# Kernel tuning notes

Hardware: AMD Instinct MI355X
Metric: run time of the kernel (lower is better)

## Reference

```python
import jax, jax.numpy as jnp
import numpy as np

# B complexes of L residues; C atom channels; K nearest neighbors
B, L, C, K = 8, 2500, 14, 9
N = B * L
E = N * K
NUM_CLASSES, EMB, HID, NL = 20, 128, 128, 3


def silu(x):
    return x * jax.nn.sigmoid(x)


def setup_inputs() -> dict:
    key = jax.random.key(0)
    ks = jax.random.split(key, 16)
    p = lambda k, shp, s=0.05: jax.random.normal(k, shp, dtype=jnp.float32) * s
    return {
        "X": jax.random.normal(ks[0], (N, C, 3), dtype=jnp.float32),
        "S": jax.random.randint(ks[1], (N,), 0, NUM_CLASSES),
        "E_tab": p(ks[2], (NUM_CLASSES, EMB)),       # residue embedding table
        "Wchan": p(ks[3], (NUM_CLASSES, C)),         # per-residue channel (atom) weights
        "Win": p(ks[4], (EMB, HID)),                 # input projection
        "Wr": p(ks[5], (NL, C * C, HID)),            # radial (channel-outer-product) projection
        "We1": p(ks[6], (NL, 3 * HID, HID)),         # edge MLP
        "be1": jnp.zeros((NL, HID), dtype=jnp.float32),
        "We2": p(ks[7], (NL, HID, HID)),
        "Wx1": p(ks[8], (NL, HID, HID)),             # coordinate-update MLP
        "Wx2": p(ks[9], (NL, HID, C), 0.01),
        "Wh1": p(ks[10], (NL, 2 * HID, HID)),        # node-update MLP
        "Wh2": p(ks[11], (NL, HID, HID)),
        "Wf1": p(ks[12], (HID, HID)),                # ffn_residue: SiLU,Linear,SiLU,Linear
        "Wf2": p(ks[13], (HID, NUM_CLASSES)),
    }


def knn_edges(X):
    # kNN graph per complex on CA (channel 1) coordinates, like _knn_edges
    pos = X[:, 1].reshape(B, L, 3)
    d2 = jnp.sum((pos[:, :, None, :] - pos[:, None, :, :]) ** 2, axis=-1)  # [B,L,L]
    d2 = d2 + jnp.eye(L, dtype=d2.dtype) * 1e9  # exclude self-edges
    _, idx = jax.lax.top_k(-d2, K)              # [B,L,K] nearest neighbors
    offs = (jnp.arange(B) * L)[:, None, None]
    dst = (idx + offs).reshape(-1)              # [E]
    src = jnp.repeat(jnp.arange(N), K)          # [E], sorted -> fast segment_sum
    return src, dst


def reference(X, S, E_tab, Wchan, Win, Wr, We1, be1, We2, Wx1, Wx2, Wh1, Wh2, Wf1, Wf2):
    src, dst = knn_edges(X)
    h = E_tab[S] @ Win                              # [N,HID]
    cw = jax.nn.softmax(Wchan[S], axis=-1)          # [N,C] channel weights
    cw_src = cw[src]                                # [E,C]
    for l in range(NL):
        xd = X[src] - X[dst]                        # [E,C,3]
        # MEAN-style channel-pair radial features
        rad = jnp.einsum("eci,edi->ecd", xd, xd).reshape(E, C * C) / C
        m = jnp.concatenate([h[src], h[dst], rad @ Wr[l]], axis=-1)
        m = silu(silu(m @ We1[l] + be1[l]) @ We2[l])           # [E,HID]
        coef = silu(m @ Wx1[l]) @ Wx2[l]                        # [E,C]
        xupd = xd * (coef * cw_src)[..., None]                  # [E,C,3]
        X = X + jax.ops.segment_sum(xupd, src, num_segments=N) / K
        aggm = jax.ops.segment_sum(m, src, num_segments=N)      # [N,HID]
        h = h + silu(jnp.concatenate([h, aggm], axis=-1) @ Wh1[l]) @ Wh2[l]
    # ffn_residue: Sequential(SiLU, Linear, SiLU, Linear)
    logits = silu(silu(h) @ Wf1) @ Wf2
    return logits, X
```

## Files before the change

### kernel.cpp

```cpp
#include <hip/hip_runtime.h>
#include <hip/hip_bf16.h>

typedef __hip_bfloat16 bf16;

constexpr int Bc  = 8;
constexpr int Lc  = 2500;
constexpr int Cc  = 14;
constexpr int Kc  = 9;
constexpr int Nn  = Bc * Lc;
constexpr int NCLS = 20;
constexpr int HID = 128;
constexpr int NL  = 3;
constexpr int CC  = Cc * Cc;
constexpr int X3  = Cc * 3;

typedef __bf16 bf16x8 __attribute__((ext_vector_type(8)));
typedef short  sh8    __attribute__((ext_vector_type(8)));
typedef float  f32x4  __attribute__((ext_vector_type(4)));

__device__ __forceinline__ float b2f(bf16 x) { return __bfloat162float(x); }
__device__ __forceinline__ float b2fu(unsigned short u) {
  return __uint_as_float(((unsigned int)u) << 16);
}
__device__ __forceinline__ unsigned short f2bu(float x) {
  bf16 h = __float2bfloat16(x);
  return *reinterpret_cast<unsigned short*>(&h);
}
__device__ __forceinline__ float siluf(float x) {
  return x * __builtin_amdgcn_rcpf(1.0f + __expf(-x));
}
__device__ __forceinline__ int clampi(int v, int n) {
  return ((unsigned)v < (unsigned)n) ? v : 0;
}
__device__ __forceinline__ void unpk2(unsigned int u, float& a, float& b) {
  a = __uint_as_float(u << 16);
  b = __uint_as_float(u & 0xffff0000u);
}

__device__ __forceinline__ f32x4 mfma16(sh8 a, sh8 b, f32x4 c) {
  return __builtin_amdgcn_mfma_f32_16x16x32_bf16(
      __builtin_bit_cast(bf16x8, a), __builtin_bit_cast(bf16x8, b), c, 0, 0, 0);
}

__device__ __forceinline__ int fragoff(int e, int k, int MT) {
  return (((k >> 5) * MT + (e >> 4)) << 9) +
         (((e & 15) + (((k >> 3) & 3) << 4)) << 3) + (k & 7);
}

__global__ __launch_bounds__(128) void wrp_kernel(const float* __restrict__ Wr,
                                                  const float* __restrict__ We1,
                                                  float* __restrict__ Wrp) {
  int l = blockIdx.x / CC, j = blockIdx.x % CC;
  int t = threadIdx.x;
  __shared__ float row[HID];
  row[t] = Wr[(size_t)(l * CC + j) * HID + t];
  __syncthreads();
  float acc = 0.f;
  #pragma unroll 4
  for (int k = 0; k < HID; ++k)
    acc += row[k] * We1[(size_t)(l * 384 + 256 + k) * HID + t];
  Wrp[(size_t)(l * CC + j) * HID + t] = acc;
}

constexpr int NSH = 26;
struct ShufArgs {
  const float* src[NSH];
  unsigned short* dst[NSH];
  int K[NSH], N[NSH], KT[NSH], NT[NSH];
};

__global__ void shufb_kernel(ShufArgs a) {
  int e = blockIdx.y;
  int K = a.K[e], N = a.N[e], NT = a.NT[e];
  int total = a.KT[e] * NT * 512;
  const float* W = a.src[e];
  unsigned short* out = a.dst[e];
  for (int idx = blockIdx.x * blockDim.x + threadIdx.x; idx < total;
       idx += gridDim.x * blockDim.x) {
    int j = idx & 7;
    int lane = (idx >> 3) & 63;
    int nt = (idx >> 9) % NT;
    int kt = idx / (512 * NT);
    int k = kt * 32 + ((lane >> 4) << 3) + j;
    int n = nt * 16 + (lane & 15);
    float v = (k < K && n < N) ? W[(size_t)k * N + n] : 0.f;
    out[idx] = f2bu(v);
  }
}

__global__ __launch_bounds__(128) void htab_kernel(const float* __restrict__ Et,
                                                   const float* __restrict__ Win,
                                                   const float* __restrict__ Wch,
                                                   float* __restrict__ Htab,
                                                   float* __restrict__ cwtab) {
  int r = blockIdx.x, t = threadIdx.x;
  __shared__ float e[HID];
  e[t] = Et[r * HID + t];
  __syncthreads();
  float acc = 0.f;
  #pragma unroll 4
  for (int k = 0; k < HID; ++k) acc += e[k] * Win[k * HID + t];
  Htab[r * HID + t] = acc;
  if (t == 0) {
    float v[Cc];
    float mx = -1e30f;
    for (int c = 0; c < Cc; ++c) { v[c] = Wch[r * Cc + c]; mx = fmaxf(mx, v[c]); }
    float s = 0.f;
    for (int c = 0; c < Cc; ++c) { v[c] = __expf(v[c] - mx); s += v[c]; }
    float inv = 1.0f / s;
    for (int c = 0; c < Cc; ++c) cwtab[r * Cc + c] = v[c] * inv;
  }
}

constexpr int PSTR = 2512;

__global__ void posx_kernel(const float* __restrict__ X, float* __restrict__ posG) {
  int total = Bc * PSTR;
  for (int i = blockIdx.x * blockDim.x + threadIdx.x; i < total;
       i += gridDim.x * blockDim.x) {
    int comp = i / PSTR, j = i - comp * PSTR;
    float x = 1e30f, y = 1e30f, z = 1e30f;
    if (j < Lc) {
      size_t g = (size_t)(comp * Lc + j) * X3;
      x = X[g + 3]; y = X[g + 4]; z = X[g + 5];
    }
    float* b = posG + (size_t)comp * 3 * PSTR;
    b[j] = x; b[PSTR + j] = y; b[2 * PSTR + j] = z;
  }
}

constexpr int KR2 = 8;
constexpr int KC2 = 80;

__global__ __launch_bounds__(256) void knn_kernel(const float* __restrict__ posG,
                                                  int* __restrict__ nbr) {
  constexpr int bpc = (Lc + KR2 - 1) / KR2;
  int comp = blockIdx.x / bpc, rb = blockIdx.x % bpc;
  int t = threadIdx.x;
  int rl = t >> 5, q = t & 31;
  int r = rb * KR2 + rl;
  const float* px = posG + (size_t)comp * 3 * PSTR;
  const float* py = px + PSTR;
  const float* pz = py + PSTR;

  float bd[Kc];
  int   bi[Kc];
  #pragma unroll
  for (int k = 0; k < Kc; ++k) { bd[k] = __int_as_float(0x7f800000); bi[k] = 0x7fffffff; }

  if (r < Lc) {
    float rx = px[r], ry = py[r], rz = pz[r];
    int c0 = q * KC2;
    int c1 = c0 + KC2; if (c1 > Lc) c1 = Lc;
    for (int i = c0; i < c1; i += 4) {
      float4 xs = *(const float4*)(px + i);
      float4 ys = *(const float4*)(py + i);
      float4 zs = *(const float4*)(pz + i);
      float d2v[4];
      {
        float dx, dy, dz;
        dx = rx - xs.x; dy = ry - ys.x; dz = rz - zs.x; d2v[0] = dx*dx + dy*dy + dz*dz;
        dx = rx - xs.y; dy = ry - ys.y; dz = rz - zs.y; d2v[1] = dx*dx + dy*dy + dz*dz;
        dx = rx - xs.z; dy = ry - ys.z; dz = rz - zs.z; d2v[2] = dx*dx + dy*dy + dz*dz;
        dx = rx - xs.w; dy = ry - ys.w; dz = rz - zs.w; d2v[3] = dx*dx + dy*dy + dz*dz;
      }
      #pragma unroll
      for (int u = 0; u < 4; ++u) {
        int ii = i + u;
        float d2 = d2v[u];
        if (ii != r && d2 < bd[Kc - 1]) {
          bd[Kc - 1] = d2; bi[Kc - 1] = ii;
          #pragma unroll
          for (int p = Kc - 1; p > 0; --p) {
            if (bd[p] < bd[p - 1]) {
              float td = bd[p]; bd[p] = bd[p - 1]; bd[p - 1] = td;
              int   ti = bi[p]; bi[p] = bi[p - 1]; bi[p - 1] = ti;
            }
          }
        }
      }
    }
  }

  int gbase = (comp * Lc + r) * Kc;
  #pragma unroll
  for (int k = 0; k < Kc; ++k) {
    unsigned long long mykey =
        ((unsigned long long)__float_as_uint(bd[0]) << 32) | (unsigned int)bi[0];
    unsigned long long w = mykey;
    #pragma unroll
    for (int m = 1; m <= 16; m <<= 1) {
      unsigned long long o = __shfl_xor(w, m);
      if (o < w) w = o;
    }
    if (r < Lc && q == k)
      nbr[gbase + k] = comp * Lc + (int)(unsigned int)(w & 0xffffffffULL);
    if (mykey == w) {
      #pragma unroll
      for (int s = 0; s < Kc - 1; ++s) { bd[s] = bd[s + 1]; bi[s] = bi[s + 1]; }
      bd[Kc - 1] = __int_as_float(0x7f800000); bi[Kc - 1] = 0x7fffffff;
    }
  }
}

__global__ __launch_bounds__(256) void nodeABm_kernel(
    const int* __restrict__ S, const float* __restrict__ Htab,
    float* __restrict__ hv,
    const unsigned short* __restrict__ We1a_s, const unsigned short* __restrict__ We1b_s,
    const float* __restrict__ be1n, bf16* __restrict__ hA, bf16* __restrict__ hB) {
  __shared__ __align__(16) unsigned short sB[4 * 512];
  int t = threadIdx.x, n0 = blockIdx.x * 16;
  int lane = t & 63, wv = t >> 6, quad = lane >> 4, l15 = lane & 15, wnb = wv << 5;

  for (int o = t; o < 16 * HID; o += 256) {
    int row = o >> 7, k = o & 127;
    float v = Htab[clampi(S[n0 + row], NCLS) * HID + k];
    hv[(size_t)(n0 + row) * HID + k] = v;
    sB[fragoff(row, k, 1)] = f2bu(v);
  }
  __syncthreads();

  f32x4 a3[2] = {{0,0,0,0},{0,0,0,0}}, a4[2] = {{0,0,0,0},{0,0,0,0}};
  const sh8* sBv = (const sh8*)sB;
  for (int kt = 0; kt < 4; ++kt) {
    sh8 a = sBv[kt * 64 + lane];
    sh8 b0 = ((const sh8*)We1a_s)[((kt << 3) + (wv << 1) + 0) * 64 + lane];
    sh8 b1 = ((const sh8*)We1a_s)[((kt << 3) + (wv << 1) + 1) * 64 + lane];
    sh8 c0 = ((const sh8*)We1b_s)[((kt << 3) + (wv << 1) + 0) * 64 + lane];
    sh8 c1 = ((const sh8*)We1b_s)[((kt << 3) + (wv << 1) + 1) * 64 + lane];
    a3[0] = mfma16(a, b0, a3[0]); a3[1] = mfma16(a, b1, a3[1]);
    a4[0] = mfma16(a, c0, a4[0]); a4[1] = mfma16(a, c1, a4[1]);
  }
  #pragma unroll
  for (int nl = 0; nl < 2; ++nl) {
    int col = wnb + (nl << 4) + l15;
    float be = be1n[col];
    #pragma unroll
    for (int r = 0; r < 4; ++r) {
      int row = (quad << 2) + r;
      hA[(size_t)(n0 + row) * HID + col] = __float2bfloat16(a3[nl][r] + be);
      hB[(size_t)(n0 + row) * HID + col] = __float2bfloat16(a4[nl][r]);
    }
  }
}

__global__ __launch_bounds__(256) void fupdAB_kernel(
    float* __restrict__ h, const bf16* __restrict__ aggm,
    const unsigned short* __restrict__ Wh1_s, const unsigned short* __restrict__ Wh2_s,
    const unsigned short* __restrict__ We1a_s, const unsigned short* __restrict__ We1b_s,
    const float* __restrict__ be1n, bf16* __restrict__ hA, bf16* __restrict__ hB) {
  __shared__ __align__(16) unsigned short sA[8 * 512];
  __shared__ __align__(16) unsigned short sB[4 * 512];
  int t = threadIdx.x, n0 = blockIdx.x * 16;
  int lane = t & 63, wv = t >> 6, quad = lane >> 4, l15 = lane & 15, wnb = wv << 5;

  for (int o = t; o < 16 * 256; o += 256) {
    int row = o >> 8, k = o & 255;
    float v = (k < HID) ? h[(size_t)(n0 + row) * HID + k]
                        : b2f(aggm[(size_t)(n0 + row) * HID + (k - HID)]);
    sA[fragoff(row, k, 1)] = f2bu(v);
  }
  __syncthreads();

  f32x4 a1[2] = {{0,0,0,0},{0,0,0,0}};
  const sh8* sAv = (const sh8*)sA;
  for (int kt = 0; kt < 8; ++kt) {
    sh8 a = sAv[kt * 64 + lane];
    sh8 b0 = ((const sh8*)Wh1_s)[((kt << 3) + (wv << 1) + 0) * 64 + lane];
    sh8 b1 = ((const sh8*)Wh1_s)[((kt << 3) + (wv << 1) + 1) * 64 + lane];
    a1[0] = mfma16(a, b0, a1[0]);
    a1[1] = mfma16(a, b1, a1[1]);
  }
  #pragma unroll
  for (int nl = 0; nl < 2; ++nl) {
    int col = wnb + (nl << 4) + l15;
    #pragma unroll
    for (int r = 0; r < 4; ++r)
      sB[fragoff((quad << 2) + r, col, 1)] = f2bu(siluf(a1[nl][r]));
  }
  __syncthreads();

  f32x4 a2[2] = {{0,0,0,0},{0,0,0,0}};
  const sh8* sBv = (const sh8*)sB;
  for (int kt = 0; kt < 4; ++kt) {
    sh8 a = sBv[kt * 64 + lane];
    sh8 b0 = ((const sh8*)Wh2_s)[((kt << 3) + (wv << 1) + 0) * 64 + lane];
    sh8 b1 = ((const sh8*)Wh2_s)[((kt << 3) + (wv << 1) + 1) * 64 + lane];
    a2[0] = mfma16(a, b0, a2[0]);
    a2[1] = mfma16(a, b1, a2[1]);
  }
  float hn[2][4];
  #pragma unroll
  for (int nl = 0; nl < 2; ++nl) {
    int col = wnb + (nl << 4) + l15;
    #pragma unroll
    for (int r = 0; r < 4; ++r) {
      int row = (quad << 2) + r;
      float v = h[(size_t)(n0 + row) * HID + col] + a2[nl][r];
      h[(size_t)(n0 + row) * HID + col] = v;
      hn[nl][r] = v;
    }
  }
  __syncthreads();
  #pragma unroll
  for (int nl = 0; nl < 2; ++nl) {
    int col = wnb + (nl << 4) + l15;
    #pragma unroll
    for (int r = 0; r < 4; ++r)
      sB[fragoff((quad << 2) + r, col, 1)] = f2bu(hn[nl][r]);
  }
  __syncthreads();

  f32x4 a3[2] = {{0,0,0,0},{0,0,0,0}}, a4[2] = {{0,0,0,0},{0,0,0,0}};
  for (int kt = 0; kt < 4; ++kt) {
    sh8 a = sBv[kt * 64 + lane];
    sh8 b0 = ((const sh8*)We1a_s)[((kt << 3) + (wv << 1) + 0) * 64 + lane];
    sh8 b1 = ((const sh8*)We1a_s)[((kt << 3) + (wv << 1) + 1) * 64 + lane];
    sh8 c0 = ((const sh8*)We1b_s)[((kt << 3) + (wv << 1) + 0) * 64 + lane];
    sh8 c1 = ((const sh8*)We1b_s)[((kt << 3) + (wv << 1) + 1) * 64 + lane];
    a3[0] = mfma16(a, b0, a3[0]); a3[1] = mfma16(a, b1, a3[1]);
    a4[0] = mfma16(a, c0, a4[0]); a4[1] = mfma16(a, c1, a4[1]);
  }
  #pragma unroll
  for (int nl = 0; nl < 2; ++nl) {
    int col = wnb + (nl << 4) + l15;
    float be = be1n[col];
    #pragma unroll
    for (int r = 0; r < 4; ++r) {
      int row = (quad << 2) + r;
      hA[(size_t)(n0 + row) * HID + col] = __float2bfloat16(a3[nl][r] + be);
      hB[(size_t)(n0 + row) * HID + col] = __float2bfloat16(a4[nl][r]);
    }
  }
}

__global__ __launch_bounds__(256) void fupdF_kernel(
    const float* __restrict__ h, const bf16* __restrict__ aggm,
    const unsigned short* __restrict__ Wh1_s, const unsigned short* __restrict__ Wh2_s,
    const unsigned short* __restrict__ Wf1_s, const unsigned short* __restrict__ Wf2_s,
    float* __restrict__ out) {
  __shared__ __align__(16) unsigned short sA[8 * 512];
  __shared__ __align__(16) unsigned short sB[4 * 512];
  int t = threadIdx.x, n0 = blockIdx.x * 16;
  int lane = t & 63, wv = t >> 6, quad = lane >> 4, l15 = lane & 15, wnb = wv << 5;

  for (int o = t; o < 16 * 256; o += 256) {
    int row = o >> 8, k = o & 255;
    float v = (k < HID) ? h[(size_t)(n0 + row) * HID + k]
                        : b2f(aggm[(size_t)(n0 + row) * HID + (k - HID)]);
    sA[fragoff(row, k, 1)] = f2bu(v);
  }
  __syncthreads();

  f32x4 a1[2] = {{0,0,0,0},{0,0,0,0}};
  const sh8* sAv = (const sh8*)sA;
  for (int kt = 0; kt < 8; ++kt) {
    sh8 a = sAv[kt * 64 + lane];
    sh8 b0 = ((const sh8*)Wh1_s)[((kt << 3) + (wv << 1) + 0) * 64 + lane];
    sh8 b1 = ((const sh8*)Wh1_s)[((kt << 3) + (wv << 1) + 1) * 64 + lane];
    a1[0] = mfma16(a, b0, a1[0]);
    a1[1] = mfma16(a, b1, a1[1]);
  }
  #pragma unroll
  for (int nl = 0; nl < 2; ++nl) {
    int col = wnb + (nl << 4) + l15;
    #pragma unroll
    for (int r = 0; r < 4; ++r)
      sB[fragoff((quad << 2) + r, col, 1)] = f2bu(siluf(a1[nl][r]));
  }
  __syncthreads();

  f32x4 a2[2] = {{0,0,0,0},{0,0,0,0}};
  const sh8* sBv = (const sh8*)sB;
  for (int kt = 0; kt < 4; ++kt) {
    sh8 a = sBv[kt * 64 + lane];
    sh8 b0 = ((const sh8*)Wh2_s)[((kt << 3) + (wv << 1) + 0) * 64 + lane];
    sh8 b1 = ((const sh8*)Wh2_s)[((kt << 3) + (wv << 1) + 1) * 64 + lane];
    a2[0] = mfma16(a, b0, a2[0]);
    a2[1] = mfma16(a, b1, a2[1]);
  }
  float u2[2][4];
  #pragma unroll
  for (int nl = 0; nl < 2; ++nl) {
    int col = wnb + (nl << 4) + l15;
    #pragma unroll
    for (int r = 0; r < 4; ++r) {
      int row = (quad << 2) + r;
      u2[nl][r] = siluf(h[(size_t)(n0 + row) * HID + col] + a2[nl][r]);
    }
  }
  __syncthreads();
  #pragma unroll
  for (int nl = 0; nl < 2; ++nl) {
    int col = wnb + (nl << 4) + l15;
    #pragma unroll
    for (int r = 0; r < 4; ++r)
      sB[fragoff((quad << 2) + r, col, 1)] = f2bu(u2[nl][r]);
  }
  __syncthreads();

  f32x4 a3[2] = {{0,0,0,0},{0,0,0,0}};
  for (int kt = 0; kt < 4; ++kt) {
    sh8 a = sBv[kt * 64 + lane];
    sh8 b0 = ((const sh8*)Wf1_s)[((kt << 3) + (wv << 1) + 0) * 64 + lane];
    sh8 b1 = ((const sh8*)Wf1_s)[((kt << 3) + (wv << 1) + 1) * 64 + lane];
    a3[0] = mfma16(a, b0, a3[0]);
    a3[1] = mfma16(a, b1, a3[1]);
  }
  #pragma unroll
  for (int nl = 0; nl < 2; ++nl) {
    int col = wnb + (nl << 4) + l15;
    #pragma unroll
    for (int r = 0; r < 4; ++r)
      sA[fragoff((quad << 2) + r, col, 1)] = f2bu(siluf(a3[nl][r]));
  }
  __syncthreads();

  if (wv < 2) {
    f32x4 a5 = {0.f, 0.f, 0.f, 0.f};
    for (int kt = 0; kt < 4; ++kt) {
      sh8 a = sAv[kt * 64 + lane];
      sh8 b = ((const sh8*)Wf2_s)[(kt * 2 + wv) * 64 + lane];
      a5 = mfma16(a, b, a5);
    }
    int col = (wv << 4) + l15;
    if (col < NCLS) {
      #pragma unroll
      for (int r = 0; r < 4; ++r) {
        int row = (quad << 2) + r;
        out[(size_t)(n0 + row) * NCLS + col] = a5[r];
      }
    }
  }
}

constexpr int GN  = 4;
constexpr int NE  = GN * Kc;
constexpr int MT3 = 3;

__global__ __launch_bounds__(256) void edge_kernel(
    const float* __restrict__ Xin, float* __restrict__ Xout,
    const bf16* __restrict__ hA, const bf16* __restrict__ hB,
    const int* __restrict__ S, const float* __restrict__ cwtab,
    const int* __restrict__ nbr,
    const unsigned short* __restrict__ Wrp_s, const unsigned short* __restrict__ We2_s,
    const unsigned short* __restrict__ Wx1_s, const unsigned short* __restrict__ Wx2_s,
    bf16* __restrict__ aggm) {
  __shared__ __align__(16) unsigned short s_R1[48 * 224];
  __shared__ __align__(16) unsigned short s_R2[48 * 128];
  __shared__ __align__(16) unsigned short s_xd[NE * 44];
  __shared__ __align__(16) unsigned short s_hA[GN * 128];
  __shared__ float s_cw[GN * Cc];
  __shared__ int   s_dst[NE];

  int t = threadIdx.x;
  int n0 = blockIdx.x * GN;
  int lane = t & 63, wv = t >> 6;
  int quad = lane >> 4, l15 = lane & 15;
  int wnb = wv << 5;

  if (t < NE) s_dst[t] = clampi(nbr[n0 * Kc + t], Nn);
  if (t >= 64 && t < 64 + GN * Cc) {
    int o = t - 64;
    s_cw[o] = cwtab[clampi(S[n0 + o / Cc], NCLS) * Cc + o % Cc];
  }
  {
    uint4* r1 = (uint4*)s_R1;
    for (int o = t; o < 1344; o += 256) r1[o] = make_uint4(0u, 0u, 0u, 0u);
    uint4* r2 = (uint4*)s_R2;
    for (int o = t; o < 768; o += 256) r2[o] = make_uint4(0u, 0u, 0u, 0u);
    const unsigned int* src = (const unsigned int*)(hA + (size_t)n0 * HID);
    unsigned int* dA = (unsigned int*)s_hA;
    for (int o = t; o < GN * 64; o += 256) dA[o] = src[o];
  }
  __syncthreads();

  unsigned short hbr[MT3][2][4];
  {
    const unsigned short* hbu = (const unsigned short*)hB;
    #pragma unroll
    for (int mt = 0; mt < MT3; ++mt)
      #pragma unroll
      for (int nl = 0; nl < 2; ++nl) {
        int col = wnb + (nl << 4) + l15;
        #pragma unroll
        for (int r = 0; r < 4; ++r) {
          int row = (mt << 4) + (quad << 2) + r;
          hbr[mt][nl][r] =
              (row < NE) ? hbu[(size_t)s_dst[row] * HID + col] : (unsigned short)0;
        }
      }
  }

  for (int o = t; o < NE * X3; o += 256) {
    int e = o / X3, i = o - e * X3;
    float v = Xin[(size_t)(n0 + e / Kc) * X3 + i] - Xin[(size_t)s_dst[e] * X3 + i];
    s_xd[e * 44 + i] = f2bu(v);
  }
  __syncthreads();

  if (t < 252) {
    int e = t / 7, jc = t - (t / 7) * 7;
    const unsigned int* xu = (const unsigned int*)(s_xd + e * 44);
    unsigned int u[21];
    #pragma unroll
    for (int i = 0; i < 21; ++i) u[i] = xu[i];
    float xdv[42];
    #pragma unroll
    for (int i = 0; i < 21; ++i) unpk2(u[i], xdv[2 * i], xdv[2 * i + 1]);
    #pragma unroll
    for (int half = 0; half < 2; ++half) {
      int c = 2 * jc + half;
      const unsigned short* xe = s_xd + e * 44;
      float xc0 = b2fu(xe[c * 3 + 0]);
      float xc1 = b2fu(xe[c * 3 + 1]);
      float xc2 = b2fu(xe[c * 3 + 2]);
      int jbase = c * Cc;
      #pragma unroll
      for (int d = 0; d < 14; ++d) {
        float v = (xc0 * xdv[d * 3 + 0] + xc1 * xdv[d * 3 + 1] +
                   xc2 * xdv[d * 3 + 2]) * (1.0f / 14.0f);
        s_R1[fragoff(e, jbase + d, MT3)] = f2bu(v);
      }
    }
  }
  __syncthreads();

  f32x4 acc1[MT3][2];
  #pragma unroll
  for (int mt = 0; mt < MT3; ++mt)
    #pragma unroll
    for (int nl = 0; nl < 2; ++nl) acc1[mt][nl] = (f32x4){0.f, 0.f, 0.f, 0.f};
  const sh8* r1v = (const sh8*)s_R1;
  for (int kt = 0; kt < 7; ++kt) {
    sh8 b0 = ((const sh8*)Wrp_s)[((kt << 3) + (wv << 1) + 0) * 64 + lane];
    sh8 b1 = ((const sh8*)Wrp_s)[((kt << 3) + (wv << 1) + 1) * 64 + lane];
    #pragma unroll
    for (int mt = 0; mt < MT3; ++mt) {
      sh8 a = r1v[(kt * MT3 + mt) * 64 + lane];
      acc1[mt][0] = mfma16(a, b0, acc1[mt][0]);
      acc1[mt][1] = mfma16(a, b1, acc1[mt][1]);
    }
  }
  #pragma unroll
  for (int mt = 0; mt < MT3; ++mt)
    #pragma unroll
    for (int nl = 0; nl < 2; ++nl) {
      int col = wnb + (nl << 4) + l15;
      #pragma unroll
      for (int r = 0; r < 4; ++r) {
        int row = (mt << 4) + (quad << 2) + r;
        if (row < NE) {
          float v = acc1[mt][nl][r] + b2fu(s_hA[((row / Kc) << 7) + col]) +
                    b2fu(hbr[mt][nl][r]);
          s_R2[fragoff(row, col, MT3)] = f2bu(siluf(v));
        }
      }
    }
  __syncthreads();

  f32x4 acc2[MT3][2];
  #pragma unroll
  for (int mt = 0; mt < MT3; ++mt)
    #pragma unroll
    for (int nl = 0; nl < 2; ++nl) acc2[mt][nl] = (f32x4){0.f, 0.f, 0.f, 0.f};
  const sh8* r2v = (const sh8*)s_R2;
  for (int kt = 0; kt < 4; ++kt) {
    sh8 b0 = ((const sh8*)We2_s)[((kt << 3) + (wv << 1) + 0) * 64 + lane];
    sh8 b1 = ((const sh8*)We2_s)[((kt << 3) + (wv << 1) + 1) * 64 + lane];
    #pragma unroll
    for (int mt = 0; mt < MT3; ++mt) {
      sh8 a = r2v[(kt * MT3 + mt) * 64 + lane];
      acc2[mt][0] = mfma16(a, b0, acc2[mt][0]);
      acc2[mt][1] = mfma16(a, b1, acc2[mt][1]);
    }
  }
  __syncthreads();
  #pragma unroll
  for (int mt = 0; mt < MT3; ++mt)
    #pragma unroll
    for (int nl = 0; nl < 2; ++nl) {
      int col = wnb + (nl << 4) + l15;
      #pragma unroll
      for (int r = 0; r < 4; ++r) {
        int row = (mt << 4) + (quad << 2) + r;
        s_R2[fragoff(row, col, MT3)] = f2bu(siluf(acc2[mt][nl][r]));
      }
    }
  __syncthreads();

  for (int o = t; o < GN * HID; o += 256) {
    int g = o >> 7, col = o & 127;
    float s = 0.f;
    #pragma unroll
    for (int k = 0; k < Kc; ++k) s += b2fu(s_R2[fragoff(g * Kc + k, col, MT3)]);
    aggm[(size_t)(n0 + g) * HID + col] = __float2bfloat16(s);
  }
  f32x4 acc3[MT3][2];
  #pragma unroll
  for (int mt = 0; mt < MT3; ++mt)
    #pragma unroll
    for (int nl = 0; nl < 2; ++nl) acc3[mt][nl] = (f32x4){0.f, 0.f, 0.f, 0.f};
  for (int kt = 0; kt < 4; ++kt) {
    sh8 b0 = ((const sh8*)Wx1_s)[((kt << 3) + (wv << 1) + 0) * 64 + lane];
    sh8 b1 = ((const sh8*)Wx1_s)[((kt << 3) + (wv << 1) + 1) * 64 + lane];
    #pragma unroll
    for (int mt = 0; mt < MT3; ++mt) {
      sh8 a = r2v[(kt * MT3 + mt) * 64 + lane];
      acc3[mt][0] = mfma16(a, b0, acc3[mt][0]);
      acc3[mt][1] = mfma16(a, b1, acc3[mt][1]);
    }
  }
  #pragma unroll
  for (int mt = 0; mt < MT3; ++mt)
    #pragma unroll
    for (int nl = 0; nl < 2; ++nl) {
      int col = wnb + (nl << 4) + l15;
      #pragma unroll
      for (int r = 0; r < 4; ++r) {
        int row = (mt << 4) + (quad << 2) + r;
        s_R1[fragoff(row, col, MT3)] = f2bu(siluf(acc3[mt][nl][r]));
      }
    }
  __syncthreads();

  float* s_coef = (float*)s_R2;
  if (wv == 0) {
    f32x4 a4[MT3];
    #pragma unroll
    for (int mt = 0; mt < MT3; ++mt) a4[mt] = (f32x4){0.f, 0.f, 0.f, 0.f};
    for (int kt = 0; kt < 4; ++kt) {
      sh8 b = ((const sh8*)Wx2_s)[kt * 64 + lane];
      #pragma unroll
      for (int mt = 0; mt < MT3; ++mt) {
        sh8 a = r1v[(kt * MT3 + mt) * 64 + lane];
        a4[mt] = mfma16(a, b, a4[mt]);
      }
    }
    #pragma unroll
    for (int mt = 0; mt < MT3; ++mt)
      #pragma unroll
      for (int r = 0; r < 4; ++r) {
        int row = (mt << 4) + (quad << 2) + r;
        s_coef[(row << 4) + l15] = a4[mt][r];
      }
  }
  __syncthreads();

  for (int o = t; o < GN * X3; o += 256) {
    int g = o / X3, rem = o - g * X3, c = rem / 3;
    float s = 0.f;
    #pragma unroll
    for (int k = 0; k < Kc; ++k) {
      int e = g * Kc + k;
      s += b2fu(s_xd[e * 44 + rem]) * s_coef[(e << 4) + c];
    }
    int gn = n0 + g;
    Xout[(size_t)gn * X3 + rem] =
        Xin[(size_t)gn * X3 + rem] + s * s_cw[g * Cc + c] * (1.0f / 9.0f);
  }
}

extern "C" void kernel_launch(void* const* d_in, const int* in_sizes, int n_in,
                              void* d_out, int out_size, void* d_ws, size_t ws_size,
                              hipStream_t stream) {
  const float* X    = (const float*)d_in[0];
  const int*   S    = (const int*)d_in[1];
  const float* Etab = (const float*)d_in[2];
  const float* Wch  = (const float*)d_in[3];
  const float* Win  = (const float*)d_in[4];
  const float* Wr   = (const float*)d_in[5];
  const float* We1  = (const float*)d_in[6];
  const float* be1  = (const float*)d_in[7];
  const float* We2  = (const float*)d_in[8];
  const float* Wx1  = (const float*)d_in[9];
  const float* Wx2  = (const float*)d_in[10];
  const float* Wh1  = (const float*)d_in[11];
  const float* Wh2  = (const float*)d_in[12];
  const float* Wf1  = (const float*)d_in[13];
  const float* Wf2  = (const float*)d_in[14];
  (void)in_sizes; (void)n_in; (void)out_size; (void)ws_size;

  char* base = (char*)d_ws;
  size_t off = 0;
  auto alloc = [&](size_t bytes) {
    void* p = base + off;
    off += (bytes + 255) & ~(size_t)255;
    return p;
  };
  int*   nbr   = (int*)  alloc((size_t)Nn * Kc * 4);
  float* Htab  = (float*)alloc(NCLS * HID * 4);
  float* cwtab = (float*)alloc(NCLS * Cc * 4);
  float* Wrpf  = (float*)alloc((size_t)NL * CC * HID * 4);
  float* posG  = (float*)alloc((size_t)Bc * 3 * PSTR * 4);
  float* Xa    = (float*)alloc((size_t)Nn * X3 * 4);
  float* Xb    = (float*)alloc((size_t)Nn * X3 * 4);
  float* hv    = (float*)alloc((size_t)Nn * HID * 4);
  bf16*  hAv   = (bf16*) alloc((size_t)Nn * HID * 2);
  bf16*  hBv   = (bf16*) alloc((size_t)Nn * HID * 2);
  bf16*  aggmv = (bf16*) alloc((size_t)Nn * HID * 2);
  constexpr int WRP_SZ = 7 * 8 * 512;
  constexpr int W128_SZ = 4 * 8 * 512;
  constexpr int WX2_SZ = 4 * 1 * 512;
  constexpr int WH1_SZ = 8 * 8 * 512;
  constexpr int WF2_SZ = 4 * 2 * 512;
  unsigned short* Wrp_s  = (unsigned short*)alloc((size_t)NL * WRP_SZ * 2);
  unsigned short* We2_s  = (unsigned short*)alloc((size_t)NL * W128_SZ * 2);
  unsigned short* Wx1_s  = (unsigned short*)alloc((size_t)NL * W128_SZ * 2);
  unsigned short* Wx2_s  = (unsigned short*)alloc((size_t)NL * WX2_SZ * 2);
  unsigned short* Wh1_s  = (unsigned short*)alloc((size_t)NL * WH1_SZ * 2);
  unsigned short* Wh2_s  = (unsigned short*)alloc((size_t)NL * W128_SZ * 2);
  unsigned short* We1a_s = (unsigned short*)alloc((size_t)NL * W128_SZ * 2);
  unsigned short* We1b_s = (unsigned short*)alloc((size_t)NL * W128_SZ * 2);
  unsigned short* Wf1_s  = (unsigned short*)alloc(W128_SZ * 2);
  unsigned short* Wf2_s  = (unsigned short*)alloc(WF2_SZ * 2);

  wrp_kernel<<<NL * CC, 128, 0, stream>>>(Wr, We1, Wrpf);
  htab_kernel<<<NCLS, 128, 0, stream>>>(Etab, Win, Wch, Htab, cwtab);
  posx_kernel<<<79, 256, 0, stream>>>(X, posG);
  knn_kernel<<<Bc * ((Lc + KR2 - 1) / KR2), 256, 0, stream>>>(posG, nbr);

  ShufArgs sa;
  for (int l = 0; l < NL; ++l) {
    int e = l * 8;
    sa.src[e+0] = Wrpf + (size_t)l * CC * HID;       sa.dst[e+0] = Wrp_s  + (size_t)l * WRP_SZ;
    sa.K[e+0] = CC;  sa.N[e+0] = HID; sa.KT[e+0] = 7; sa.NT[e+0] = 8;
    sa.src[e+1] = We2 + (size_t)l * HID * HID;       sa.dst[e+1] = We2_s  + (size_t)l * W128_SZ;
    sa.K[e+1] = HID; sa.N[e+1] = HID; sa.KT[e+1] = 4; sa.NT[e+1] = 8;
    sa.src[e+2] = Wx1 + (size_t)l * HID * HID;       sa.dst[e+2] = Wx1_s  + (size_t)l * W128_SZ;
    sa.K[e+2] = HID; sa.N[e+2] = HID; sa.KT[e+2] = 4; sa.NT[e+2] = 8;
    sa.src[e+3] = Wx2 + (size_t)l * HID * Cc;        sa.dst[e+3] = Wx2_s  + (size_t)l * WX2_SZ;
    sa.K[e+3] = HID; sa.N[e+3] = Cc;  sa.KT[e+3] = 4; sa.NT[e+3] = 1;
    sa.src[e+4] = Wh1 + (size_t)l * 256 * HID;       sa.dst[e+4] = Wh1_s  + (size_t)l * WH1_SZ;
    sa.K[e+4] = 256; sa.N[e+4] = HID; sa.KT[e+4] = 8; sa.NT[e+4] = 8;
    sa.src[e+5] = Wh2 + (size_t)l * HID * HID;       sa.dst[e+5] = Wh2_s  + (size_t)l * W128_SZ;
    sa.K[e+5] = HID; sa.N[e+5] = HID; sa.KT[e+5] = 4; sa.NT[e+5] = 8;
    sa.src[e+6] = We1 + (size_t)l * 384 * HID;       sa.dst[e+6] = We1a_s + (size_t)l * W128_SZ;
    sa.K[e+6] = HID; sa.N[e+6] = HID; sa.KT[e+6] = 4; sa.NT[e+6] = 8;
    sa.src[e+7] = We1 + (size_t)l * 384 * HID + (size_t)HID * HID;
    sa.dst[e+7] = We1b_s + (size_t)l * W128_SZ;
    sa.K[e+7] = HID; sa.N[e+7] = HID; sa.KT[e+7] = 4; sa.NT[e+7] = 8;
  }
  sa.src[24] = Wf1; sa.dst[24] = Wf1_s; sa.K[24] = HID; sa.N[24] = HID;
  sa.KT[24] = 4; sa.NT[24] = 8;
  sa.src[25] = Wf2; sa.dst[25] = Wf2_s; sa.K[25] = HID; sa.N[25] = NCLS;
  sa.KT[25] = 4; sa.NT[25] = 2;
  shufb_kernel<<<dim3(16, NSH), 256, 0, stream>>>(sa);

  nodeABm_kernel<<<Nn / 16, 256, 0, stream>>>(S, Htab, hv, We1a_s, We1b_s, be1,
                                              hAv, hBv);

  float* out = (float*)d_out;
  float* outX = out + (size_t)Nn * NCLS;
  const float* Xi = X;
  for (int l = 0; l < NL; ++l) {
    float* Xo = (l == NL - 1) ? outX : ((l == 0) ? Xb : Xa);
    edge_kernel<<<Nn / GN, 256, 0, stream>>>(
        Xi, Xo, hAv, hBv, S, cwtab, nbr,
        Wrp_s + (size_t)l * WRP_SZ, We2_s + (size_t)l * W128_SZ,
        Wx1_s + (size_t)l * W128_SZ, Wx2_s + (size_t)l * WX2_SZ, aggmv);
    if (l < NL - 1) {
      fupdAB_kernel<<<Nn / 16, 256, 0, stream>>>(
          hv, aggmv, Wh1_s + (size_t)l * WH1_SZ, Wh2_s + (size_t)l * W128_SZ,
          We1a_s + (size_t)(l + 1) * W128_SZ, We1b_s + (size_t)(l + 1) * W128_SZ,
          be1 + (l + 1) * HID, hAv, hBv);
    } else {
      fupdF_kernel<<<Nn / 16, 256, 0, stream>>>(
          hv, aggmv, Wh1_s + (size_t)l * WH1_SZ, Wh2_s + (size_t)l * W128_SZ,
          Wf1_s, Wf2_s, out);
    }
    Xi = Xo;
  }
}
```

Baseline: 498.2 us.

## Split radial-feature GEMM into two K-halves to shrink LDS; widen kNN per-row lanes

The edge kernel's radial buffer s_R1 is cut from 224 to 128 K-columns. The channel-pair features are now built in two passes (channels 0-8, then 9-13), each followed by its MFMA accumulation, and the Wrp weights are repacked to a padded 256-row layout to match. The aim is lower LDS use per block so more blocks fit per CU, at the cost of extra barriers, a second zeroing pass and a padded K dimension. The kNN kernel separately moves to 4 rows per block with 64 lanes per row, giving each lane a shorter candidate scan but adding one more shuffle-reduction step.

```diff
diff --git a/kernel.cpp b/kernel.cpp
--- a/kernel.cpp
+++ b/kernel.cpp
@@ -50,8 +50,17 @@
 __global__ __launch_bounds__(128) void wrp_kernel(const float* __restrict__ Wr,
                                                   const float* __restrict__ We1,
                                                   float* __restrict__ Wrp) {
-  int l = blockIdx.x / CC, j = blockIdx.x % CC;
+  int l = blockIdx.x >> 8, m = blockIdx.x & 255;
   int t = threadIdx.x;
+  int c = 0, d = 0;
+  bool real = false;
+  if (m < 126) { c = m / 14; d = m - c * 14; real = true; }
+  else if (m >= 128 && m < 198) {
+    int mm = m - 128;
+    c = 9 + mm / 14; d = mm - (mm / 14) * 14; real = true;
+  }
+  if (!real) { Wrp[(size_t)(l * 256 + m) * HID + t] = 0.f; return; }
+  int j = c * Cc + d;
   __shared__ float row[HID];
   row[t] = Wr[(size_t)(l * CC + j) * HID + t];
   __syncthreads();
@@ -59,7 +68,7 @@
   #pragma unroll 4
   for (int k = 0; k < HID; ++k)
     acc += row[k] * We1[(size_t)(l * 384 + 256 + k) * HID + t];
-  Wrp[(size_t)(l * CC + j) * HID + t] = acc;
+  Wrp[(size_t)(l * 256 + m) * HID + t] = acc;
 }
 
 constexpr int NSH = 26;
@@ -129,15 +138,15 @@
   }
 }
 
-constexpr int KR2 = 8;
-constexpr int KC2 = 80;
+constexpr int KR2 = 4;
+constexpr int KC2 = 40;
 
 __global__ __launch_bounds__(256) void knn_kernel(const float* __restrict__ posG,
                                                   int* __restrict__ nbr) {
   constexpr int bpc = (Lc + KR2 - 1) / KR2;
   int comp = blockIdx.x / bpc, rb = blockIdx.x % bpc;
   int t = threadIdx.x;
-  int rl = t >> 5, q = t & 31;
+  int rl = t >> 6, q = t & 63;
   int r = rb * KR2 + rl;
   const float* px = posG + (size_t)comp * 3 * PSTR;
   const float* py = px + PSTR;
@@ -189,7 +198,7 @@
         ((unsigned long long)__float_as_uint(bd[0]) << 32) | (unsigned int)bi[0];
     unsigned long long w = mykey;
     #pragma unroll
-    for (int m = 1; m <= 16; m <<= 1) {
+    for (int m = 1; m <= 32; m <<= 1) {
       unsigned long long o = __shfl_xor(w, m);
       if (o < w) w = o;
     }
@@ -446,7 +455,7 @@
     const unsigned short* __restrict__ Wrp_s, const unsigned short* __restrict__ We2_s,
     const unsigned short* __restrict__ Wx1_s, const unsigned short* __restrict__ Wx2_s,
     bf16* __restrict__ aggm) {
-  __shared__ __align__(16) unsigned short s_R1[48 * 224];
+  __shared__ __align__(16) unsigned short s_R1[48 * 128];
   __shared__ __align__(16) unsigned short s_R2[48 * 128];
   __shared__ __align__(16) unsigned short s_xd[NE * 44];
   __shared__ __align__(16) unsigned short s_hA[GN * 128];
@@ -466,7 +475,7 @@
   }
   {
     uint4* r1 = (uint4*)s_R1;
-    for (int o = t; o < 1344; o += 256) r1[o] = make_uint4(0u, 0u, 0u, 0u);
+    for (int o = t; o < 768; o += 256) r1[o] = make_uint4(0u, 0u, 0u, 0u);
     uint4* r2 = (uint4*)s_R2;
     for (int o = t; o < 768; o += 256) r2[o] = make_uint4(0u, 0u, 0u, 0u);
     const unsigned int* src = (const unsigned int*)(hA + (size_t)n0 * HID);
@@ -499,8 +508,8 @@
   }
   __syncthreads();
 
-  if (t < 252) {
-    int e = t / 7, jc = t - (t / 7) * 7;
+  if (t < 180) {
+    int e = t / 5, jc = t - (t / 5) * 5;
     const unsigned int* xu = (const unsigned int*)(s_xd + e * 44);
     unsigned int u[21];
     #pragma unroll
@@ -508,19 +517,21 @@
     float xdv[42];
     #pragma unroll
     for (int i = 0; i < 21; ++i) unpk2(u[i], xdv[2 * i], xdv[2 * i + 1]);
+    const unsigned short* xe = s_xd + e * 44;
     #pragma unroll
     for (int half = 0; half < 2; ++half) {
       int c = 2 * jc + half;
-      const unsigned short* xe = s_xd + e * 44;
-      float xc0 = b2fu(xe[c * 3 + 0]);
-      float xc1 = b2fu(xe[c * 3 + 1]);
-      float xc2 = b2fu(xe[c * 3 + 2]);
-      int jbase = c * Cc;
-      #pragma unroll
-      for (int d = 0; d < 14; ++d) {
-        float v = (xc0 * xdv[d * 3 + 0] + xc1 * xdv[d * 3 + 1] +
-                   xc2 * xdv[d * 3 + 2]) * (1.0f / 14.0f);
-        s_R1[fragoff(e, jbase + d, MT3)] = f2bu(v);
+      if (c <= 8) {
+        float xc0 = b2fu(xe[c * 3 + 0]);
+        float xc1 = b2fu(xe[c * 3 + 1]);
+        float xc2 = b2fu(xe[c * 3 + 2]);
+        int jbase = c * Cc;
+        #pragma unroll
+        for (int d = 0; d < 14; ++d) {
+          float v = (xc0 * xdv[d * 3 + 0] + xc1 * xdv[d * 3 + 1] +
+                     xc2 * xdv[d * 3 + 2]) * (1.0f / 14.0f);
+          s_R1[fragoff(e, jbase + d, MT3)] = f2bu(v);
+        }
       }
     }
   }
@@ -532,12 +543,45 @@
     #pragma unroll
     for (int nl = 0; nl < 2; ++nl) acc1[mt][nl] = (f32x4){0.f, 0.f, 0.f, 0.f};
   const sh8* r1v = (const sh8*)s_R1;
-  for (int kt = 0; kt < 7; ++kt) {
+  for (int kt = 0; kt < 4; ++kt) {
     sh8 b0 = ((const sh8*)Wrp_s)[((kt << 3) + (wv << 1) + 0) * 64 + lane];
     sh8 b1 = ((const sh8*)Wrp_s)[((kt << 3) + (wv << 1) + 1) * 64 + lane];
     #pragma unroll
     for (int mt = 0; mt < MT3; ++mt) {
       sh8 a = r1v[(kt * MT3 + mt) * 64 + lane];
+      acc1[mt][0] = mfma16(a, b0, acc1[mt][0]);
+      acc1[mt][1] = mfma16(a, b1, acc1[mt][1]);
+    }
+  }
+  __syncthreads();
+  {
+    uint4* r1z = (uint4*)s_R1;
+    for (int o = t; o < 768; o += 256) r1z[o] = make_uint4(0u, 0u, 0u, 0u);
+  }
+  __syncthreads();
+
+  for (int o = t; o < NE * Cc; o += 256) {
+    int e = o / Cc, d = o - (o / Cc) * Cc;
+    const unsigned short* xe = s_xd + e * 44;
+    float xd0 = b2fu(xe[d * 3 + 0]);
+    float xd1 = b2fu(xe[d * 3 + 1]);
+    float xd2 = b2fu(xe[d * 3 + 2]);
+    #pragma unroll
+    for (int ci = 0; ci < 5; ++ci) {
+      int c = 9 + ci;
+      float v = (b2fu(xe[c * 3 + 0]) * xd0 + b2fu(xe[c * 3 + 1]) * xd1 +
+                 b2fu(xe[c * 3 + 2]) * xd2) * (1.0f / 14.0f);
+      s_R1[fragoff(e, ci * Cc + d, MT3)] = f2bu(v);
+    }
+  }
+  __syncthreads();
+
+  for (int kt = 4; kt < 8; ++kt) {
+    sh8 b0 = ((const sh8*)Wrp_s)[((kt << 3) + (wv << 1) + 0) * 64 + lane];
+    sh8 b1 = ((const sh8*)Wrp_s)[((kt << 3) + (wv << 1) + 1) * 64 + lane];
+    #pragma unroll
+    for (int mt = 0; mt < MT3; ++mt) {
+      sh8 a = r1v[((kt - 4) * MT3 + mt) * 64 + lane];
       acc1[mt][0] = mfma16(a, b0, acc1[mt][0]);
       acc1[mt][1] = mfma16(a, b1, acc1[mt][1]);
     }
@@ -611,6 +655,7 @@
       acc3[mt][1] = mfma16(a, b1, acc3[mt][1]);
     }
   }
+  __syncthreads();
   #pragma unroll
   for (int mt = 0; mt < MT3; ++mt)
     #pragma unroll
@@ -691,7 +736,7 @@
   int*   nbr   = (int*)  alloc((size_t)Nn * Kc * 4);
   float* Htab  = (float*)alloc(NCLS * HID * 4);
   float* cwtab = (float*)alloc(NCLS * Cc * 4);
-  float* Wrpf  = (float*)alloc((size_t)NL * CC * HID * 4);
+  float* Wrpf  = (float*)alloc((size_t)NL * 256 * HID * 4);
   float* posG  = (float*)alloc((size_t)Bc * 3 * PSTR * 4);
   float* Xa    = (float*)alloc((size_t)Nn * X3 * 4);
   float* Xb    = (float*)alloc((size_t)Nn * X3 * 4);
@@ -699,7 +744,7 @@
   bf16*  hAv   = (bf16*) alloc((size_t)Nn * HID * 2);
   bf16*  hBv   = (bf16*) alloc((size_t)Nn * HID * 2);
   bf16*  aggmv = (bf16*) alloc((size_t)Nn * HID * 2);
-  constexpr int WRP_SZ = 7 * 8 * 512;
+  constexpr int WRP_SZ = 8 * 8 * 512;
   constexpr int W128_SZ = 4 * 8 * 512;
   constexpr int WX2_SZ = 4 * 1 * 512;
   constexpr int WH1_SZ = 8 * 8 * 512;
@@ -715,7 +760,7 @@
   unsigned short* Wf1_s  = (unsigned short*)alloc(W128_SZ * 2);
   unsigned short* Wf2_s  = (unsigned short*)alloc(WF2_SZ * 2);
 
-  wrp_kernel<<<NL * CC, 128, 0, stream>>>(Wr, We1, Wrpf);
+  wrp_kernel<<<NL * 256, 128, 0, stream>>>(Wr, We1, Wrpf);
   htab_kernel<<<NCLS, 128, 0, stream>>>(Etab, Win, Wch, Htab, cwtab);
   posx_kernel<<<79, 256, 0, stream>>>(X, posG);
   knn_kernel<<<Bc * ((Lc + KR2 - 1) / KR2), 256, 0, stream>>>(posG, nbr);
@@ -723,8 +768,8 @@
   ShufArgs sa;
   for (int l = 0; l < NL; ++l) {
     int e = l * 8;
-    sa.src[e+0] = Wrpf + (size_t)l * CC * HID;       sa.dst[e+0] = Wrp_s  + (size_t)l * WRP_SZ;
-    sa.K[e+0] = CC;  sa.N[e+0] = HID; sa.KT[e+0] = 7; sa.NT[e+0] = 8;
+    sa.src[e+0] = Wrpf + (size_t)l * 256 * HID;      sa.dst[e+0] = Wrp_s  + (size_t)l * WRP_SZ;
+    sa.K[e+0] = 256; sa.N[e+0] = HID; sa.KT[e+0] = 8; sa.NT[e+0] = 8;
     sa.src[e+1] = We2 + (size_t)l * HID * HID;       sa.dst[e+1] = We2_s  + (size_t)l * W128_SZ;
     sa.K[e+1] = HID; sa.N[e+1] = HID; sa.KT[e+1] = 4; sa.NT[e+1] = 8;
     sa.src[e+2] = Wx1 + (size_t)l * HID * HID;       sa.dst[e+2] = Wx1_s  + (size_t)l * W128_SZ;
```

Result: slower. 557.0 us (+11.8%).
